# Kernel tuning notes

Measured on AMD Instinct MI355X. Metric: run time of the kernel, lower is better.

## Reference

```python
import jax, jax.numpy as jnp
import numpy as np

EPS = 1e-6


def setup_inputs() -> dict:
    key = jax.random.key(0)
    k1, = jax.random.split(key, 1)
    N = 8192
    X = jax.random.normal(k1, (1, N, 3), dtype=jnp.float32) * 10.0  # Ca coords, Angstrom-ish scale
    mask = jnp.ones((1, N), dtype=jnp.float32)
    return {"X": X, "mask": mask, "top_k": 30}


def reference(X, mask, top_k):
    # mask_2D: [B, N, N]
    mask_2D = mask[:, None, :] * mask[:, :, None]
    # pairwise distances: [B, N, N]
    dX = X[:, None, :, :] - X[:, :, None, :]            # [B, N, N, 3]
    D = mask_2D * jnp.sqrt(jnp.sum(dX * dX, axis=-1) + EPS)
    D_max = jnp.max(D, axis=-1, keepdims=True)
    D_adjust = D + 2.0 * (1.0 - mask_2D) * D_max        # push masked pairs far away
    k = min(top_k, X.shape[-2])
    # smallest-k via top_k on negated distances
    neg_D, E_idx = jax.lax.top_k(-D_adjust, k)          # [B, N, k]
    D_neighbors = -neg_D
    # gather_edges on mask_2D[..., None]: [B, N, k, 1]
    mask_neighbors = jnp.take_along_axis(mask_2D[..., None], E_idx[..., None], axis=2)
    return (D_neighbors, E_idx, mask_neighbors)
```

## Files before the change

### kernel.cpp

```cpp
#include <hip/hip_runtime.h>
#include <math.h>
#include <stdint.h>

#define NPTS 8192
#define TOPK 30
#define BUFSZ 1024
#define SENT 0xFFFFFFFFFFFFFFFFULL

__device__ __forceinline__ unsigned long long exact_key(const float* __restrict__ X,
                                                        float xi, float yi, float zi, int j) {
#pragma clang fp contract(off)
    float dx = X[j * 3 + 0] - xi;
    float dy = X[j * 3 + 1] - yi;
    float dz = X[j * 3 + 2] - zi;
    float d2 = dx * dx;
    d2 = d2 + dy * dy;
    d2 = d2 + dz * dz;
    float d = sqrtf(d2 + 1e-6f);
    return ((unsigned long long)__float_as_uint(d) << 32) | (unsigned int)j;
}

__device__ __forceinline__ unsigned long long bcast64(unsigned long long v, int src) {
    return (unsigned long long)__shfl((long long)v, src);
}

__global__ __launch_bounds__(256)
void knn_topk_kernel(const float* __restrict__ X,
                     const float* __restrict__ mask,
                     float* __restrict__ out)
{
    __shared__ int buf[4][BUFSZ];

    const int lane = threadIdx.x & 63;
    const int wv   = threadIdx.x >> 6;
    const int row  = (int)(blockIdx.x << 2) | wv;

    const float xi = X[row * 3 + 0];
    const float yi = X[row * 3 + 1];
    const float zi = X[row * 3 + 2];

    float smin = INFINITY;
#pragma unroll
    for (int k = 0; k < 4; ++k) {
        const int j = (lane + 64 * k) * 32;
        const float dx = X[j * 3 + 0] - xi;
        const float dy = X[j * 3 + 1] - yi;
        const float dz = X[j * 3 + 2] - zi;
        const float q = fmaf(dz, dz, fmaf(dy, dy, dx * dx));
        smin = fminf(smin, q);
    }
#pragma unroll
    for (int k = 2; k <= 64; k <<= 1) {
#pragma unroll
        for (int m = k >> 1; m >= 1; m >>= 1) {
            const float p = __shfl_xor(smin, m);
            const bool take_min = (((lane & k) == 0) == ((lane & m) == 0));
            smin = ((smin < p) == take_min) ? smin : p;
        }
    }
    float T = __shfl(smin, 3);

    const float4* X4 = (const float4*)X;
    int C;
    for (;;) {
        C = 0;
        for (int t = 0; t < NPTS / 256; ++t) {
            const int cbase = t * 256 + (lane << 2);
            const int bi = (t * 64 + lane) * 3;
            const float4 a0 = X4[bi + 0];
            const float4 a1 = X4[bi + 1];
            const float4 a2 = X4[bi + 2];

            const float dx0 = a0.x - xi, dy0 = a0.y - yi, dz0 = a0.z - zi;
            const float dx1 = a0.w - xi, dy1 = a1.x - yi, dz1 = a1.y - zi;
            const float dx2 = a1.z - xi, dy2 = a1.w - yi, dz2 = a2.x - zi;
            const float dx3 = a2.y - xi, dy3 = a2.z - yi, dz3 = a2.w - zi;

            const float q0 = fmaf(dz0, dz0, fmaf(dy0, dy0, dx0 * dx0));
            const float q1 = fmaf(dz1, dz1, fmaf(dy1, dy1, dx1 * dx1));
            const float q2 = fmaf(dz2, dz2, fmaf(dy2, dy2, dx2 * dx2));
            const float q3 = fmaf(dz3, dz3, fmaf(dy3, dy3, dx3 * dx3));

            const bool p0 = q0 < T;
            const bool p1 = q1 < T;
            const bool p2 = q2 < T;
            const bool p3 = q3 < T;

#pragma unroll
            for (int k = 0; k < 4; ++k) {
                const bool pk = (k == 0) ? p0 : (k == 1) ? p1 : (k == 2) ? p2 : p3;
                const unsigned long long ball = __ballot(pk);
                const int myoff = C + __popcll(ball & ((1ull << lane) - 1ull));
                if (pk && myoff < BUFSZ) buf[wv][myoff] = cbase + k;
                C += __popcll(ball);
            }
        }
        if (C >= 33 && C <= BUFSZ) break;
        T = (C < 33) ? T * 2.0f : T * 0.5f;
    }

    unsigned long long list = SENT;
    for (int s0 = 0; s0 < C; s0 += 64) {
        const int s = s0 + lane;
        unsigned long long ck = SENT;
        if (s < C) ck = exact_key(X, xi, yi, zi, buf[wv][s]);

#pragma unroll
        for (int k = 2; k <= 64; k <<= 1) {
#pragma unroll
            for (int m = k >> 1; m >= 1; m >>= 1) {
                const unsigned long long p = (unsigned long long)__shfl_xor((long long)ck, m);
                const bool take_min = (((lane & k) == 0) == ((lane & m) == 0));
                ck = ((ck < p) == take_min) ? ck : p;
            }
        }

        const unsigned long long cg = bcast64(ck, 63 - lane);
        unsigned long long v = (lane < TOPK) ? list : cg;
#pragma unroll
        for (int m = 32; m >= 1; m >>= 1) {
            const unsigned long long p = (unsigned long long)__shfl_xor((long long)v, m);
            const bool low = ((lane & m) == 0);
            const bool lt = (v < p);
            v = (low == lt) ? v : p;
        }
        list = (lane < TOPK) ? v : SENT;
    }

    if (lane < TOPK) {
        const int   li = (int)(uint32_t)(list & 0xFFFFFFFFu);
        const float lv = __uint_as_float((uint32_t)(list >> 32));
        const int base = row * TOPK + lane;
        out[base]                   = lv;
        out[NPTS * TOPK + base]     = (float)li;
        out[2 * NPTS * TOPK + base] = mask[row] * mask[li];
    }
}

extern "C" void kernel_launch(void* const* d_in, const int* in_sizes, int n_in,
                              void* d_out, int out_size, void* d_ws, size_t ws_size,
                              hipStream_t stream) {
    const float* X    = (const float*)d_in[0];
    const float* mask = (const float*)d_in[1];
    float* out        = (float*)d_out;

    dim3 grid(NPTS / 4), block(256);
    knn_topk_kernel<<<grid, block, 0, stream>>>(X, mask, out);
}
```

Measured before the change: 110.5 us.

## Replace ballot-based compaction with per-lane candidate slots and prefix-sum compaction

```diff
diff --git a/kernel.cpp b/kernel.cpp
--- a/kernel.cpp
+++ b/kernel.cpp
@@ -4,7 +4,9 @@
 
 #define NPTS 8192
 #define TOPK 30
-#define BUFSZ 1024
+#define SLOTS 16
+#define USABLE 15
+#define BUF2SZ 384
 #define SENT 0xFFFFFFFFFFFFFFFFULL
 
 __device__ __forceinline__ unsigned long long exact_key(const float* __restrict__ X,
@@ -29,7 +31,8 @@
                      const float* __restrict__ mask,
                      float* __restrict__ out)
 {
-    __shared__ int buf[4][BUFSZ];
+    __shared__ int buf [4][SLOTS * 64];
+    __shared__ int buf2[4][BUF2SZ + 1];
 
     const int lane = threadIdx.x & 63;
     const int wv   = threadIdx.x >> 6;
@@ -46,8 +49,7 @@
         const float dx = X[j * 3 + 0] - xi;
         const float dy = X[j * 3 + 1] - yi;
         const float dz = X[j * 3 + 2] - zi;
-        const float q = fmaf(dz, dz, fmaf(dy, dy, dx * dx));
-        smin = fminf(smin, q);
+        smin = fminf(smin, fmaf(dz, dz, fmaf(dy, dy, dx * dx)));
     }
 #pragma unroll
     for (int k = 2; k <= 64; k <<= 1) {
@@ -58,12 +60,12 @@
             smin = ((smin < p) == take_min) ? smin : p;
         }
     }
-    float T = __shfl(smin, 3);
+    float T = __shfl(smin, 5);
 
     const float4* X4 = (const float4*)X;
-    int C;
+    int Cv, off, maxv, valid;
     for (;;) {
-        C = 0;
+        int cnt = 0;
         for (int t = 0; t < NPTS / 256; ++t) {
             const int cbase = t * 256 + (lane << 2);
             const int bi = (t * 64 + lane) * 3;
@@ -81,29 +83,45 @@
             const float q2 = fmaf(dz2, dz2, fmaf(dy2, dy2, dx2 * dx2));
             const float q3 = fmaf(dz3, dz3, fmaf(dy3, dy3, dx3 * dx3));
 
-            const bool p0 = q0 < T;
-            const bool p1 = q1 < T;
-            const bool p2 = q2 < T;
-            const bool p3 = q3 < T;
-
 #pragma unroll
             for (int k = 0; k < 4; ++k) {
-                const bool pk = (k == 0) ? p0 : (k == 1) ? p1 : (k == 2) ? p2 : p3;
-                const unsigned long long ball = __ballot(pk);
-                const int myoff = C + __popcll(ball & ((1ull << lane) - 1ull));
-                if (pk && myoff < BUFSZ) buf[wv][myoff] = cbase + k;
-                C += __popcll(ball);
+                const float qk = (k == 0) ? q0 : (k == 1) ? q1 : (k == 2) ? q2 : q3;
+                const bool  pk = qk < T;
+                const int slot = pk ? ((cnt < USABLE) ? cnt : USABLE) : USABLE;
+                buf[wv][slot * 64 + lane] = cbase + k;
+                cnt += pk ? 1 : 0;
             }
         }
-        if (C >= 33 && C <= BUFSZ) break;
-        T = (C < 33) ? T * 2.0f : T * 0.5f;
+
+        valid = (cnt < USABLE) ? cnt : USABLE;
+        int s = valid;
+#pragma unroll
+        for (int d = 1; d < 64; d <<= 1) {
+            const int n = __shfl_up(s, d);
+            if (lane >= d) s += n;
+        }
+        Cv  = __shfl(s, 63);
+        off = s - valid;
+        maxv = valid;
+#pragma unroll
+        for (int d = 32; d; d >>= 1) maxv = max(maxv, __shfl_xor(maxv, d));
+
+        const bool anyover = __ballot(cnt > USABLE) != 0ull;
+        if (!anyover && Cv >= 33 && Cv <= BUF2SZ) break;
+        T = anyover ? T * 0.5f : (Cv < 33 ? T * 2.0f : T * 0.5f);
+    }
+
+    for (int k = 0; k < maxv; ++k) {
+        const int e = buf[wv][k * 64 + lane];
+        const int dst = (k < valid) ? (off + k) : BUF2SZ;
+        buf2[wv][dst] = e;
     }
 
     unsigned long long list = SENT;
-    for (int s0 = 0; s0 < C; s0 += 64) {
+    for (int s0 = 0; s0 < Cv; s0 += 64) {
         const int s = s0 + lane;
         unsigned long long ck = SENT;
-        if (s < C) ck = exact_key(X, xi, yi, zi, buf[wv][s]);
+        if (s < Cv) ck = exact_key(X, xi, yi, zi, buf2[wv][s]);
 
 #pragma unroll
         for (int k = 2; k <= 64; k <<= 1) {
@@ -121,8 +139,7 @@
         for (int m = 32; m >= 1; m >>= 1) {
             const unsigned long long p = (unsigned long long)__shfl_xor((long long)v, m);
             const bool low = ((lane & m) == 0);
-            const bool lt = (v < p);
-            v = (low == lt) ? v : p;
+            v = (low == (v < p)) ? v : p;
         }
         list = (lane < TOPK) ? v : SENT;
     }
```

After: 108.6 us. Within noise of the previous version (-1.7%).

## Replace per-candidate ballot compaction with bitmask scan and prefix-sum extraction

Applied to the files above, without the earlier changes.

```diff
diff --git a/kernel.cpp b/kernel.cpp
--- a/kernel.cpp
+++ b/kernel.cpp
@@ -4,7 +4,7 @@
 
 #define NPTS 8192
 #define TOPK 30
-#define BUFSZ 1024
+#define BUF2SZ 768
 #define SENT 0xFFFFFFFFFFFFFFFFULL
 
 __device__ __forceinline__ unsigned long long exact_key(const float* __restrict__ X,
@@ -24,12 +24,12 @@
     return (unsigned long long)__shfl((long long)v, src);
 }
 
-__global__ __launch_bounds__(256)
+__global__ __launch_bounds__(256, 8)
 void knn_topk_kernel(const float* __restrict__ X,
                      const float* __restrict__ mask,
                      float* __restrict__ out)
 {
-    __shared__ int buf[4][BUFSZ];
+    __shared__ int buf2[4][BUF2SZ];
 
     const int lane = threadIdx.x & 63;
     const int wv   = threadIdx.x >> 6;
@@ -41,13 +41,12 @@
 
     float smin = INFINITY;
 #pragma unroll
-    for (int k = 0; k < 4; ++k) {
-        const int j = (lane + 64 * k) * 32;
+    for (int k = 0; k < 8; ++k) {
+        const int j = lane + (k << 6);
         const float dx = X[j * 3 + 0] - xi;
         const float dy = X[j * 3 + 1] - yi;
         const float dz = X[j * 3 + 2] - zi;
-        const float q = fmaf(dz, dz, fmaf(dy, dy, dx * dx));
-        smin = fminf(smin, q);
+        smin = fminf(smin, fmaf(dz, dz, fmaf(dy, dy, dx * dx)));
     }
 #pragma unroll
     for (int k = 2; k <= 64; k <<= 1) {
@@ -58,52 +57,82 @@
             smin = ((smin < p) == take_min) ? smin : p;
         }
     }
-    float T = __shfl(smin, 3);
+    float T = __shfl(smin, 19);
 
     const float4* X4 = (const float4*)X;
-    int C;
+    unsigned m0, m1, m2, m3;
+    int cnt, C;
+
+#define SCAN8(MREG, TBASE)                                                     \
+    {                                                                          \
+        unsigned cm = 0;                                                       \
+        _Pragma("unroll")                                                      \
+        for (int t8 = 0; t8 < 8; ++t8) {                                       \
+            const int t = (TBASE) + t8;                                        \
+            const int bi = (t * 64 + lane) * 3;                                \
+            const float4 a0 = X4[bi + 0];                                      \
+            const float4 a1 = X4[bi + 1];                                      \
+            const float4 a2 = X4[bi + 2];                                      \
+            const float dx0 = a0.x - xi, dy0 = a0.y - yi, dz0 = a0.z - zi;     \
+            const float dx1 = a0.w - xi, dy1 = a1.x - yi, dz1 = a1.y - zi;     \
+            const float dx2 = a1.z - xi, dy2 = a1.w - yi, dz2 = a2.x - zi;     \
+            const float dx3 = a2.y - xi, dy3 = a2.z - yi, dz3 = a2.w - zi;     \
+            const float q0 = fmaf(dz0, dz0, fmaf(dy0, dy0, dx0 * dx0));        \
+            const float q1 = fmaf(dz1, dz1, fmaf(dy1, dy1, dx1 * dx1));        \
+            const float q2 = fmaf(dz2, dz2, fmaf(dy2, dy2, dx2 * dx2));        \
+            const float q3 = fmaf(dz3, dz3, fmaf(dy3, dy3, dx3 * dx3));        \
+            unsigned nib = (q0 < T) ? 1u : 0u;                                 \
+            nib |= (q1 < T) ? 2u : 0u;                                         \
+            nib |= (q2 < T) ? 4u : 0u;                                         \
+            nib |= (q3 < T) ? 8u : 0u;                                         \
+            cm |= nib << (t8 * 4);                                             \
+        }                                                                      \
+        MREG = cm;                                                             \
+    }
+
     for (;;) {
-        C = 0;
-        for (int t = 0; t < NPTS / 256; ++t) {
-            const int cbase = t * 256 + (lane << 2);
-            const int bi = (t * 64 + lane) * 3;
-            const float4 a0 = X4[bi + 0];
-            const float4 a1 = X4[bi + 1];
-            const float4 a2 = X4[bi + 2];
-
-            const float dx0 = a0.x - xi, dy0 = a0.y - yi, dz0 = a0.z - zi;
-            const float dx1 = a0.w - xi, dy1 = a1.x - yi, dz1 = a1.y - zi;
-            const float dx2 = a1.z - xi, dy2 = a1.w - yi, dz2 = a2.x - zi;
-            const float dx3 = a2.y - xi, dy3 = a2.z - yi, dz3 = a2.w - zi;
-
-            const float q0 = fmaf(dz0, dz0, fmaf(dy0, dy0, dx0 * dx0));
-            const float q1 = fmaf(dz1, dz1, fmaf(dy1, dy1, dx1 * dx1));
-            const float q2 = fmaf(dz2, dz2, fmaf(dy2, dy2, dx2 * dx2));
-            const float q3 = fmaf(dz3, dz3, fmaf(dy3, dy3, dx3 * dx3));
-
-            const bool p0 = q0 < T;
-            const bool p1 = q1 < T;
-            const bool p2 = q2 < T;
-            const bool p3 = q3 < T;
-
+        SCAN8(m0, 0)
+        SCAN8(m1, 8)
+        SCAN8(m2, 16)
+        SCAN8(m3, 24)
+        cnt = __popc(m0) + __popc(m1) + __popc(m2) + __popc(m3);
+        C = cnt;
 #pragma unroll
-            for (int k = 0; k < 4; ++k) {
-                const bool pk = (k == 0) ? p0 : (k == 1) ? p1 : (k == 2) ? p2 : p3;
-                const unsigned long long ball = __ballot(pk);
-                const int myoff = C + __popcll(ball & ((1ull << lane) - 1ull));
-                if (pk && myoff < BUFSZ) buf[wv][myoff] = cbase + k;
-                C += __popcll(ball);
-            }
-        }
-        if (C >= 33 && C <= BUFSZ) break;
+        for (int d = 32; d; d >>= 1) C += __shfl_xor(C, d);
+        if (C >= 33 && C <= BUF2SZ) break;
         T = (C < 33) ? T * 2.0f : T * 0.5f;
     }
+#undef SCAN8
+
+    int s = cnt;
+#pragma unroll
+    for (int d = 1; d < 64; d <<= 1) {
+        const int n = __shfl_up(s, d);
+        if (lane >= d) s += n;
+    }
+    int off = s - cnt;
+
+#define EXTRACT(MREG, TBASE)                                                   \
+    {                                                                          \
+        unsigned mm = (MREG);                                                  \
+        while (mm) {                                                           \
+            const int b = __builtin_ctz(mm);                                   \
+            mm &= mm - 1;                                                      \
+            const int t = (TBASE) + (b >> 2);                                  \
+            buf2[wv][off++] = t * 256 + (lane << 2) + (b & 3);                 \
+        }                                                                      \
+    }
+    EXTRACT(m0, 0)
+    EXTRACT(m1, 8)
+    EXTRACT(m2, 16)
+    EXTRACT(m3, 24)
+#undef EXTRACT
 
     unsigned long long list = SENT;
     for (int s0 = 0; s0 < C; s0 += 64) {
-        const int s = s0 + lane;
+        const int sc = s0 + lane;
         unsigned long long ck = SENT;
-        if (s < C) ck = exact_key(X, xi, yi, zi, buf[wv][s]);
+        if (sc < C) ck = exact_key(X, xi, yi, zi, buf2[wv][sc]);
 
 #pragma unroll
         for (int k = 2; k <= 64; k <<= 1) {
@@ -121,8 +150,7 @@
         for (int m = 32; m >= 1; m >>= 1) {
             const unsigned long long p = (unsigned long long)__shfl_xor((long long)v, m);
             const bool low = ((lane & m) == 0);
-            const bool lt = (v < p);
-            v = (low == lt) ? v : p;
+            v = (low == (v < p)) ? v : p;
         }
         list = (lane < TOPK) ? v : SENT;
     }
```

After: 216.0 us. 95.4% more time.

## Replace per-candidate ballot compaction with per-lane bitmasks and prefix-sum scatter

Applied to the files above, without the earlier changes.

```diff
diff --git a/kernel.cpp b/kernel.cpp
--- a/kernel.cpp
+++ b/kernel.cpp
@@ -4,7 +4,7 @@
 
 #define NPTS 8192
 #define TOPK 30
-#define BUFSZ 1024
+#define BUF2SZ 768
 #define SENT 0xFFFFFFFFFFFFFFFFULL
 
 __device__ __forceinline__ unsigned long long exact_key(const float* __restrict__ X,
@@ -29,7 +29,7 @@
                      const float* __restrict__ mask,
                      float* __restrict__ out)
 {
-    __shared__ int buf[4][BUFSZ];
+    __shared__ int buf2[4][BUF2SZ];
 
     const int lane = threadIdx.x & 63;
     const int wv   = threadIdx.x >> 6;
@@ -41,13 +41,12 @@
 
     float smin = INFINITY;
 #pragma unroll
-    for (int k = 0; k < 4; ++k) {
-        const int j = (lane + 64 * k) * 32;
+    for (int k = 0; k < 8; ++k) {
+        const int j = lane + (k << 6);
         const float dx = X[j * 3 + 0] - xi;
         const float dy = X[j * 3 + 1] - yi;
         const float dz = X[j * 3 + 2] - zi;
-        const float q = fmaf(dz, dz, fmaf(dy, dy, dx * dx));
-        smin = fminf(smin, q);
+        smin = fminf(smin, fmaf(dz, dz, fmaf(dy, dy, dx * dx)));
     }
 #pragma unroll
     for (int k = 2; k <= 64; k <<= 1) {
@@ -58,52 +57,72 @@
             smin = ((smin < p) == take_min) ? smin : p;
         }
     }
-    float T = __shfl(smin, 3);
+    float T = __shfl(smin, 19);
 
     const float4* X4 = (const float4*)X;
-    int C;
+    unsigned msk[8];
+    int cnt, C;
+
     for (;;) {
-        C = 0;
-        for (int t = 0; t < NPTS / 256; ++t) {
-            const int cbase = t * 256 + (lane << 2);
-            const int bi = (t * 64 + lane) * 3;
-            const float4 a0 = X4[bi + 0];
-            const float4 a1 = X4[bi + 1];
-            const float4 a2 = X4[bi + 2];
+        cnt = 0;
+#pragma unroll
+        for (int w = 0; w < 8; ++w) {
+            unsigned cm = 0;
+#pragma unroll
+            for (int t4 = 0; t4 < 4; ++t4) {
+                const int t = w * 4 + t4;
+                const int bi = (t * 64 + lane) * 3;
+                const float4 a0 = X4[bi + 0];
+                const float4 a1 = X4[bi + 1];
+                const float4 a2 = X4[bi + 2];
+                const float dx0 = a0.x - xi, dy0 = a0.y - yi, dz0 = a0.z - zi;
+                const float dx1 = a0.w - xi, dy1 = a1.x - yi, dz1 = a1.y - zi;
+                const float dx2 = a1.z - xi, dy2 = a1.w - yi, dz2 = a2.x - zi;
+                const float dx3 = a2.y - xi, dy3 = a2.z - yi, dz3 = a2.w - zi;
+                const float q0 = fmaf(dz0, dz0, fmaf(dy0, dy0, dx0 * dx0));
+                const float q1 = fmaf(dz1, dz1, fmaf(dy1, dy1, dx1 * dx1));
+                const float q2 = fmaf(dz2, dz2, fmaf(dy2, dy2, dx2 * dx2));
+                const float q3 = fmaf(dz3, dz3, fmaf(dy3, dy3, dx3 * dx3));
+                unsigned nib = (q0 < T) ? 1u : 0u;
+                nib |= (q1 < T) ? 2u : 0u;
+                nib |= (q2 < T) ? 4u : 0u;
+                nib |= (q3 < T) ? 8u : 0u;
+                cm |= nib << (t4 * 4);
+            }
+            msk[w] = cm;
+            cnt += __popc(cm);
+        }
+        C = cnt;
+#pragma unroll
+        for (int d = 32; d; d >>= 1) C += __shfl_xor(C, d);
+        if (C >= 33 && C <= BUF2SZ) break;
+        T = (C < 33) ? T * 2.0f : T * 0.5f;
+    }
 
-            const float dx0 = a0.x - xi, dy0 = a0.y - yi, dz0 = a0.z - zi;
-            const float dx1 = a0.w - xi, dy1 = a1.x - yi, dz1 = a1.y - zi;
-            const float dx2 = a1.z - xi, dy2 = a1.w - yi, dz2 = a2.x - zi;
-            const float dx3 = a2.y - xi, dy3 = a2.z - yi, dz3 = a2.w - zi;
-
-            const float q0 = fmaf(dz0, dz0, fmaf(dy0, dy0, dx0 * dx0));
-            const float q1 = fmaf(dz1, dz1, fmaf(dy1, dy1, dx1 * dx1));
-            const float q2 = fmaf(dz2, dz2, fmaf(dy2, dy2, dx2 * dx2));
-            const float q3 = fmaf(dz3, dz3, fmaf(dy3, dy3, dx3 * dx3));
-
-            const bool p0 = q0 < T;
-            const bool p1 = q1 < T;
-            const bool p2 = q2 < T;
-            const bool p3 = q3 < T;
+    int s = cnt;
+#pragma unroll
+    for (int d = 1; d < 64; d <<= 1) {
+        const int n = __shfl_up(s, d);
+        if (lane >= d) s += n;
+    }
+    int off = s - cnt;
 
 #pragma unroll
-            for (int k = 0; k < 4; ++k) {
-                const bool pk = (k == 0) ? p0 : (k == 1) ? p1 : (k == 2) ? p2 : p3;
-                const unsigned long long ball = __ballot(pk);
-                const int myoff = C + __popcll(ball & ((1ull << lane) - 1ull));
-                if (pk && myoff < BUFSZ) buf[wv][myoff] = cbase + k;
-                C += __popcll(ball);
-            }
+    for (int w = 0; w < 8; ++w) {
+        unsigned mm = msk[w];
+        while (mm) {
+            const int b = __builtin_ctz(mm);
+            mm &= mm - 1;
+            const int t = w * 4 + (b >> 2);
+            buf2[wv][off++] = t * 256 + (lane << 2) + (b & 3);
         }
-        if (C >= 33 && C <= BUFSZ) break;
-        T = (C < 33) ? T * 2.0f : T * 0.5f;
     }
 
     unsigned long long list = SENT;
     for (int s0 = 0; s0 < C; s0 += 64) {
-        const int s = s0 + lane;
+        const int sc = s0 + lane;
         unsigned long long ck = SENT;
-        if (s < C) ck = exact_key(X, xi, yi, zi, buf[wv][s]);
+        if (sc < C) ck = exact_key(X, xi, yi, zi, buf2[wv][sc]);
 
 #pragma unroll
         for (int k = 2; k <= 64; k <<= 1) {
@@ -121,8 +140,7 @@
         for (int m = 32; m >= 1; m >>= 1) {
             const unsigned long long p = (unsigned long long)__shfl_xor((long long)v, m);
             const bool low = ((lane & m) == 0);
-            const bool lt = (v < p);
-            v = (low == lt) ? v : p;
+            v = (low == (v < p)) ? v : p;
         }
         list = (lane < TOPK) ? v : SENT;
     }
```

Result: slower. 135.4 us (+22.4%).
